# Performance work log

Measured on AMD Instinct MI355X. Metric: run time of the kernel, lower is better.

The kernel has to match this reference:

```python
import jax, jax.numpy as jnp
import numpy as np

MARGIN = 2.0
EPS = 1e-6  # F.pairwise_distance default: norm of (x1 - x2 + eps)

N, D = 4096, 768


def setup_inputs() -> dict:
    key = jax.random.key(0)
    k1, k2, k3 = jax.random.split(key, 3)
    image_embedding = jax.random.normal(k1, (N, D), dtype=jnp.float32)
    text_embedding = jax.random.normal(k2, (N, D), dtype=jnp.float32)
    ground_truth = jax.random.randint(k3, (N, N), 0, 2, dtype=jnp.int32)
    return {
        "image_embedding": image_embedding,
        "text_embedding": text_embedding,
        "ground_truth": ground_truth,
    }


def reference(image_embedding, text_embedding, ground_truth):
    d = image_embedding.shape[1]
    # Pairwise squared distance with pairwise_distance's +eps on the diff:
    # ||a - b + eps||^2 = ||a||^2 + ||b||^2 - 2 a.b + 2 eps (sum a - sum b) + d eps^2
    sa = jnp.sum(image_embedding * image_embedding, axis=1)   # [n]
    sb = jnp.sum(text_embedding * text_embedding, axis=1)     # [n]
    dot = image_embedding @ text_embedding.T                  # [n, n]
    ra = jnp.sum(image_embedding, axis=1)                     # [n]
    rb = jnp.sum(text_embedding, axis=1)                      # [n]
    sq = (sa[:, None] + sb[None, :] - 2.0 * dot
          + 2.0 * EPS * (ra[:, None] - rb[None, :]) + d * EPS * EPS)
    dist = jnp.sqrt(jnp.maximum(sq, 0.0))                     # [n, n]
    label = ground_truth.astype(dist.dtype)
    hinge = jnp.maximum(MARGIN - dist, 0.0)
    loss = jnp.mean((1.0 - label) * dist * dist + label * hinge * hinge)
    return loss
```

## Files before the change

kernel.cpp:

```cpp
#include <hip/hip_runtime.h>
#include <hip/hip_bf16.h>
#include <stdint.h>
#include <stddef.h>


#define NROWS 4096
#define DIM   768
#define BM    128
#define BN    128
#define BKE   128
#define MARGIN 2.0f
#define EPSV   1e-6f

typedef float f32x4 __attribute__((ext_vector_type(4)));
typedef long  lng2  __attribute__((ext_vector_type(2)));
typedef unsigned long long u64;
typedef unsigned char fp8_t;


__global__ __launch_bounds__(256) void prologue_kernel(
    const float* __restrict__ A, const float* __restrict__ B,
    const int* __restrict__ gt,
    fp8_t* __restrict__ Af8, fp8_t* __restrict__ Bf8,
    float* __restrict__ sa, float* __restrict__ sb,
    float* __restrict__ ra, float* __restrict__ rb,
    u64* __restrict__ gtp, float* __restrict__ out)
{
    const int tid  = threadIdx.x;
    const int wave = tid >> 6;
    const int lane = tid & 63;
    const int bx   = blockIdx.x;

    if (bx == 0 && tid == 0) out[0] = 0.0f;

    if (bx < 2048) {
        const int isB  = bx >= 1024;
        const int row  = (bx & 1023) * 4 + wave;
        const float* X = isB ? B : A;
        fp8_t* Xb      = isB ? Bf8 : Af8;
        float* sdst    = isB ? sb : sa;
        float* rdst    = isB ? rb : ra;

        const float4* xr = (const float4*)(X + (size_t)row * DIM);
        unsigned int* xb = (unsigned int*)(Xb + (size_t)row * DIM);

        float sum = 0.0f, sq = 0.0f;
        #pragma unroll
        for (int jb = 0; jb < 3; ++jb) {
            float4 v = xr[lane + 64 * jb];
            int pk = 0;
            pk = __builtin_amdgcn_cvt_pk_fp8_f32(v.x, v.y, pk, false);
            pk = __builtin_amdgcn_cvt_pk_fp8_f32(v.z, v.w, pk, true);
            const int e4  = lane + 64 * jb;
            const int seg = e4 >> 5;
            const int e   = (e4 & 31) * 4;
            const int kk  = e >> 5;
            const int q   = (e >> 3) & 3;
            const int jj  = e & 7;
            const int pos = ((kk >> 1) * 4 + q) * 16 + (kk & 1) * 8 + jj;
            xb[seg * 32 + (pos >> 2)] = (unsigned int)pk;
            sum += (v.x + v.y) + (v.z + v.w);
            sq  += v.x * v.x + v.y * v.y + v.z * v.z + v.w * v.w;
        }
        #pragma unroll
        for (int off = 32; off > 0; off >>= 1) {
            sum += __shfl_down(sum, off);
            sq  += __shfl_down(sq,  off);
        }
        if (lane == 0) { rdst[row] = sum; sdst[row] = sq; }
    } else {
        const int wid = (bx - 2048) * 4 + wave;
        const size_t base = (size_t)wid * 8;
        int v[8];
        #pragma unroll
        for (int i = 0; i < 8; ++i)
            v[i] = gt[base * 64 + (size_t)i * 64 + lane];
        u64 mine = 0;
        #pragma unroll
        for (int i = 0; i < 8; ++i) {
            const u64 m = __ballot(v[i] != 0);
            if (lane == i) mine = m;
        }
        if (lane < 8) gtp[base + lane] = mine;
    }
}

__global__ __launch_bounds__(256, 4) void loss_kernel(
    const fp8_t* __restrict__ A, const fp8_t* __restrict__ B,
    const float* __restrict__ sa, const float* __restrict__ sb,
    const float* __restrict__ ra, const float* __restrict__ rb,
    const uint2* __restrict__ gtp, float* __restrict__ out)
{
    __shared__ __align__(16) fp8_t As[BM * BKE];
    __shared__ __align__(16) fp8_t Bs[BN * BKE];

    const int tid  = threadIdx.x;
    const int wave = tid >> 6;
    const int lane = tid & 63;
    const int m0 = blockIdx.y * BM;
    const int n0 = blockIdx.x * BN;

    f32x4 acc[4][4] = {};

    const int fr = lane & 15;
    const int q  = lane >> 4;
    const int wm = (wave >> 1) * 64;
    const int wn = (wave & 1) * 64;

    const int srow = lane >> 3;
    const int sp   = lane & 7;

    for (int k0 = 0; k0 < DIM; k0 += BKE) {
        __syncthreads();
        #pragma unroll
        for (int j = 0; j < 4; ++j) {
            const int c0  = wave * 256 + j * 64;
            const int row = (c0 >> 3) + srow;
            const int gcx = sp ^ (row & 7);
            const fp8_t* ga = A + (size_t)(m0 + row) * DIM + k0 + gcx * 16;
            __builtin_amdgcn_global_load_lds(
                (const __attribute__((address_space(1))) void*)ga,
                (__attribute__((address_space(3))) void*)(As + c0 * 16),
                16, 0, 0);
        }
        #pragma unroll
        for (int j = 0; j < 4; ++j) {
            const int c0  = wave * 256 + j * 64;
            const int row = (c0 >> 3) + srow;
            const int gcx = sp ^ (row & 7);
            const fp8_t* gb = B + (size_t)(n0 + row) * DIM + k0 + gcx * 16;
            __builtin_amdgcn_global_load_lds(
                (const __attribute__((address_space(1))) void*)gb,
                (__attribute__((address_space(3))) void*)(Bs + c0 * 16),
                16, 0, 0);
        }
        __syncthreads();

        #pragma unroll
        for (int kk2 = 0; kk2 < 2; ++kk2) {
            const int c = kk2 * 4 + q;
            lng2 ap[4], bp[4];
            #pragma unroll
            for (int i = 0; i < 4; ++i) {
                const int ar = wm + i * 16 + fr;
                const int br = wn + i * 16 + fr;
                ap[i] = *(const lng2*)(As + ar * BKE + ((c ^ (ar & 7)) * 16));
                bp[i] = *(const lng2*)(Bs + br * BKE + ((c ^ (br & 7)) * 16));
            }
            #pragma unroll
            for (int mi = 0; mi < 4; ++mi)
                #pragma unroll
                for (int ni = 0; ni < 4; ++ni)
                    acc[mi][ni] = __builtin_amdgcn_mfma_f32_16x16x32_fp8_fp8(
                        ap[mi][0], bp[ni][0], acc[mi][ni], 0, 0, 0);
            #pragma unroll
            for (int mi = 0; mi < 4; ++mi)
                #pragma unroll
                for (int ni = 0; ni < 4; ++ni)
                    acc[mi][ni] = __builtin_amdgcn_mfma_f32_16x16x32_fp8_fp8(
                        ap[mi][1], bp[ni][1], acc[mi][ni], 0, 0, 0);
        }
    }

    const int cq = lane & 15;
    const int rq = (lane >> 4) * 4;
    const int cb = (n0 + wn) >> 6;

    float cc[4];
    #pragma unroll
    for (int ni = 0; ni < 4; ++ni) {
        const int col = n0 + wn + ni * 16 + cq;
        cc[ni] = sb[col] - 2.0f * EPSV * rb[col];
    }

    float local = 0.0f;
    #pragma unroll
    for (int mi = 0; mi < 4; ++mi) {
        #pragma unroll
        for (int rr = 0; rr < 4; ++rr) {
            const int row = m0 + wm + mi * 16 + rq + rr;
            const float crr = sa[row] + 2.0f * EPSV * ra[row]
                            + (float)DIM * EPSV * EPSV;
            const uint2 w = gtp[(size_t)row * (NROWS / 64) + cb];
            #pragma unroll
            for (int ni = 0; ni < 4; ++ni) {
                const float d2 = (crr + cc[ni]) - 2.0f * acc[mi][ni][rr];
                const unsigned wd = (ni < 2) ? w.x : w.y;
                const float gf = (float)((wd >> (cq + (ni & 1) * 16)) & 1u);
                float contrib = d2 - gf * d2;
                if (__builtin_expect(d2 < 4.0f, 0)) {
                    const float d2c  = fmaxf(d2, 0.0f);
                    const float dist = sqrtf(d2c);
                    const float h    = fmaxf(MARGIN - dist, 0.0f);
                    contrib = (1.0f - gf) * d2c + gf * h * h;
                }
                local += contrib;
            }
        }
    }

    #pragma unroll
    for (int off = 32; off > 0; off >>= 1) local += __shfl_down(local, off);

    float* redp = (float*)As;
    __syncthreads();
    if (lane == 0) redp[wave] = local;
    __syncthreads();
    if (tid == 0) {
        const float s = (redp[0] + redp[1]) + (redp[2] + redp[3]);
        atomicAdd(out, s * (1.0f / (4096.0f * 4096.0f)));
    }
}

extern "C" void kernel_launch(void* const* d_in, const int* in_sizes, int n_in,
                              void* d_out, int out_size, void* d_ws, size_t ws_size,
                              hipStream_t stream)
{
    const float* A  = (const float*)d_in[0];
    const float* B  = (const float*)d_in[1];
    const int*   gt = (const int*)d_in[2];
    float* out = (float*)d_out;

    char* ws = (char*)d_ws;
    const size_t NB8 = (size_t)NROWS * DIM;
    fp8_t* Af8 = (fp8_t*)(ws);
    fp8_t* Bf8 = (fp8_t*)(ws + NB8);
    float* sa = (float*)(ws + 2 * NB8);
    float* sb = (float*)(ws + 2 * NB8 + 16384);
    float* ra = (float*)(ws + 2 * NB8 + 32768);
    float* rb = (float*)(ws + 2 * NB8 + 49152);
    u64* gtp  = (u64*)(ws + 2 * NB8 + 65536);

    prologue_kernel<<<dim3(10240), 256, 0, stream>>>(
        A, B, gt, Af8, Bf8, sa, sb, ra, rb, gtp, out);
    loss_kernel<<<dim3(NROWS / BN, NROWS / BM), 256, 0, stream>>>(
        Af8, Bf8, sa, sb, ra, rb, (const uint2*)gtp, out);
}
```

Baseline: 136.0 us.

## Use gfx950 scaled 16x16x128 FP8 MFMA with plain row-major FP8 layout

Replaces the 16x16x32 FP8 MFMA sequence with the gfx950 mfma_scale_f32_16x16x128_f8f6f4 instruction, using unit scales (0x7F exponent), so each 128-wide K tile is covered by one MFMA per output fragment instead of four. The prologue now writes FP8 rows in natural order instead of the permuted layout the old fragment loads needed, and each lane reads two swizzled 16-byte chunks per operand. It cuts MFMA issue count and fragment-load overhead. Occupancy hint drops from 4 to 3 blocks because of the wider operand registers. The risk is correctness if the lane-to-K mapping of the new instruction does not match the chunk loads.

```diff
diff --git a/kernel.cpp b/kernel.cpp
--- a/kernel.cpp
+++ b/kernel.cpp
@@ -13,10 +13,10 @@
 #define EPSV   1e-6f
 
 typedef float f32x4 __attribute__((ext_vector_type(4)));
-typedef long  lng2  __attribute__((ext_vector_type(2)));
+typedef int   i32x4 __attribute__((ext_vector_type(4)));
+typedef int   i32x8 __attribute__((ext_vector_type(8)));
 typedef unsigned long long u64;
 typedef unsigned char fp8_t;
-
 
 __global__ __launch_bounds__(256) void prologue_kernel(
     const float* __restrict__ A, const float* __restrict__ B,
@@ -51,14 +51,7 @@
             int pk = 0;
             pk = __builtin_amdgcn_cvt_pk_fp8_f32(v.x, v.y, pk, false);
             pk = __builtin_amdgcn_cvt_pk_fp8_f32(v.z, v.w, pk, true);
-            const int e4  = lane + 64 * jb;
-            const int seg = e4 >> 5;
-            const int e   = (e4 & 31) * 4;
-            const int kk  = e >> 5;
-            const int q   = (e >> 3) & 3;
-            const int jj  = e & 7;
-            const int pos = ((kk >> 1) * 4 + q) * 16 + (kk & 1) * 8 + jj;
-            xb[seg * 32 + (pos >> 2)] = (unsigned int)pk;
+            xb[lane + 64 * jb] = (unsigned int)pk;
             sum += (v.x + v.y) + (v.z + v.w);
             sq  += v.x * v.x + v.y * v.y + v.z * v.z + v.w * v.w;
         }
@@ -85,7 +78,7 @@
     }
 }
 
-__global__ __launch_bounds__(256, 4) void loss_kernel(
+__global__ __launch_bounds__(256, 3) void loss_kernel(
     const fp8_t* __restrict__ A, const fp8_t* __restrict__ B,
     const float* __restrict__ sa, const float* __restrict__ sb,
     const float* __restrict__ ra, const float* __restrict__ rb,
@@ -136,29 +129,27 @@
         }
         __syncthreads();
 
-        #pragma unroll
-        for (int kk2 = 0; kk2 < 2; ++kk2) {
-            const int c = kk2 * 4 + q;
-            lng2 ap[4], bp[4];
-            #pragma unroll
-            for (int i = 0; i < 4; ++i) {
-                const int ar = wm + i * 16 + fr;
-                const int br = wn + i * 16 + fr;
-                ap[i] = *(const lng2*)(As + ar * BKE + ((c ^ (ar & 7)) * 16));
-                bp[i] = *(const lng2*)(Bs + br * BKE + ((c ^ (br & 7)) * 16));
-            }
+        i32x8 af[4];
+        #pragma unroll
+        for (int i = 0; i < 4; ++i) {
+            const int ar = wm + i * 16 + fr;
+            const i32x4 lo = *(const i32x4*)(As + ar * BKE + (((2 * q)     ^ (ar & 7)) * 16));
+            const i32x4 hi = *(const i32x4*)(As + ar * BKE + (((2 * q + 1) ^ (ar & 7)) * 16));
+            af[i] = (i32x8){lo[0], lo[1], lo[2], lo[3], hi[0], hi[1], hi[2], hi[3]};
+        }
+        #pragma unroll
+        for (int ni = 0; ni < 4; ++ni) {
+            const int br = wn + ni * 16 + fr;
+            const i32x4 lo = *(const i32x4*)(Bs + br * BKE + (((2 * q)     ^ (br & 7)) * 16));
+            const i32x4 hi = *(const i32x4*)(Bs + br * BKE + (((2 * q + 1) ^ (br & 7)) * 16));
+            const i32x8 bf = (i32x8){lo[0], lo[1], lo[2], lo[3], hi[0], hi[1], hi[2], hi[3]};
             #pragma unroll
             for (int mi = 0; mi < 4; ++mi)
-                #pragma unroll
-                for (int ni = 0; ni < 4; ++ni)
-                    acc[mi][ni] = __builtin_amdgcn_mfma_f32_16x16x32_fp8_fp8(
-                        ap[mi][0], bp[ni][0], acc[mi][ni], 0, 0, 0);
-            #pragma unroll
-            for (int mi = 0; mi < 4; ++mi)
-                #pragma unroll
-                for (int ni = 0; ni < 4; ++ni)
-                    acc[mi][ni] = __builtin_amdgcn_mfma_f32_16x16x32_fp8_fp8(
-                        ap[mi][1], bp[ni][1], acc[mi][ni], 0, 0, 0);
+                acc[mi][ni] = __builtin_amdgcn_mfma_scale_f32_16x16x128_f8f6f4(
+                    af[mi], bf, acc[mi][ni],
+                    0, 0,
+                    0, 0x7F7F7F7F,
+                    0, 0x7F7F7F7F);
         }
     }
 
```

After: 254.2 us. 1.87x slower.
